# Kernel tuning notes

Measured on AMD Instinct MI355X. Metric: run time of the kernel, lower is better.

## Reference

```python
import jax, jax.numpy as jnp
import numpy as np

TEMPERATURE = 0.07
EPS = 1e-12  # matches torch F.normalize eps
B, D = 16384, 128


def setup_inputs() -> dict:
    key = jax.random.key(0)
    k1, k2 = jax.random.split(key)
    anchor = jax.random.normal(k1, (B, D), dtype=jnp.float32)
    positive = jax.random.normal(k2, (B, D), dtype=jnp.float32)
    return {"anchor": anchor, "positive": positive}


def _l2_normalize(x):
    # torch F.normalize: x / max(||x||, eps)
    n = jnp.sqrt(jnp.sum(x * x, axis=-1, keepdims=True))
    return x / jnp.maximum(n, EPS)


def reference(anchor, positive):
    a = _l2_normalize(anchor)          # [B, D]
    p = _l2_normalize(positive)        # [B, D]
    pos_sim = jnp.sum(a * p, axis=-1) / TEMPERATURE            # [B]
    sim = jnp.matmul(a, p.T) / TEMPERATURE                     # [B, B]
    neg_inf = jnp.finfo(sim.dtype).min
    bsz = sim.shape[0]
    eye = jnp.eye(bsz, dtype=bool)
    neg_sim = jnp.where(eye, neg_inf, sim)                     # diag masked
    logits = jnp.concatenate([pos_sim[:, None], neg_sim], axis=1)  # [B, B+1]
    # cross-entropy with label 0: -log_softmax(logits)[:, 0]
    lse = jax.nn.logsumexp(logits, axis=1)
    loss = lse - logits[:, 0]
    return jnp.mean(loss)
```

## Files before the change

kernel.cpp:

```cpp
#include <hip/hip_runtime.h>
#include <stdint.h>

#define NROWS 16384
#define DIM 128

typedef __attribute__((ext_vector_type(8))) __bf16 bf16x8;
typedef __attribute__((ext_vector_type(4))) float f32x4;
typedef __attribute__((ext_vector_type(4))) unsigned int u32x4;

constexpr float TEMP_INV = 1.0f / 0.07f;
constexpr float LOG2E = 1.4426950408889634f;
constexpr float LN2 = 0.69314718055994531f;
constexpr float KAPPA = LOG2E * TEMP_INV;
constexpr float SQRT_KAPPA = 4.53981600f;

__device__ __forceinline__ ushort f2bf(float x) {
  uint32_t u = __builtin_bit_cast(uint32_t, x);
  uint32_t r = (u + 0x7fffu + ((u >> 16) & 1u)) >> 16;
  return (ushort)r;
}

__device__ __forceinline__ void gload_lds16(const void* g, void* l) {
  __builtin_amdgcn_global_load_lds(
      (const __attribute__((address_space(1))) unsigned int*)g,
      (__attribute__((address_space(3))) unsigned int*)l, 16, 0, 0);
}

__global__ __launch_bounds__(256) void prep_kernel(
    const float* __restrict__ anchor, const float* __restrict__ positive,
    ushort* __restrict__ abar, ushort* __restrict__ pbar,
    float* __restrict__ pos_u)
{
  const int tid = threadIdx.x;
  const int row = blockIdx.x * 16 + (tid >> 4);
  const int c0 = (tid & 15) * 8;

  const float4* a4 = reinterpret_cast<const float4*>(anchor + (size_t)row * DIM + c0);
  const float4* p4 = reinterpret_cast<const float4*>(positive + (size_t)row * DIM + c0);
  float4 a0 = a4[0], a1 = a4[1];
  float4 p0 = p4[0], p1 = p4[1];

  float af[8] = {a0.x, a0.y, a0.z, a0.w, a1.x, a1.y, a1.z, a1.w};
  float pf[8] = {p0.x, p0.y, p0.z, p0.w, p1.x, p1.y, p1.z, p1.w};

  float sa = 0.f, sp = 0.f, dp = 0.f;
#pragma unroll
  for (int j = 0; j < 8; ++j) {
    sa += af[j] * af[j];
    sp += pf[j] * pf[j];
    dp += af[j] * pf[j];
  }
#pragma unroll
  for (int m = 1; m <= 8; m <<= 1) {
    sa += __shfl_xor(sa, m, 64);
    sp += __shfl_xor(sp, m, 64);
    dp += __shfl_xor(dp, m, 64);
  }
  float inva = 1.0f / fmaxf(sqrtf(sa), 1e-12f);
  float invp = 1.0f / fmaxf(sqrtf(sp), 1e-12f);
  float ca = inva * SQRT_KAPPA;
  float cp = invp * SQRT_KAPPA;

  ushort ua[8], up[8];
#pragma unroll
  for (int j = 0; j < 8; ++j) {
    ua[j] = f2bf(af[j] * ca);
    up[j] = f2bf(pf[j] * cp);
  }
  *reinterpret_cast<uint4*>(abar + (size_t)row * DIM + c0) = *reinterpret_cast<uint4*>(ua);
  *reinterpret_cast<uint4*>(pbar + (size_t)row * DIM + c0) = *reinterpret_cast<uint4*>(up);

  if ((tid & 15) == 0)
    pos_u[row] = dp * inva * invp * KAPPA;
}

#define NSPLIT 16
#define BM 256
#define CPB (NROWS / NSPLIT)
#define BN 32
#define NIT (CPB / BN)
#define NBUF 4
#define TILE_B (BN * 256)

__global__ __launch_bounds__(256, 4) void lse_kernel(
    const ushort* __restrict__ abar,
    const ushort* __restrict__ pbar,
    float* __restrict__ sbuf )
{
  __shared__ alignas(16) char lds[NBUF][TILE_B];

  const int tid = threadIdx.x;
  const int l = tid & 63;
  const int w = tid >> 6;
  const int r15 = l & 15;
  const int hi = l >> 4;

  const int bid = blockIdx.x;
  const int csplit = bid & 15;
  const int rowblk = bid >> 4;
  const int row0 = rowblk * BM + w * 64;
  const int col0 = csplit * CPB;

  const char* abase = (const char*)abar;
  const char* pbase = (const char*)pbar;

  bf16x8 afrag[4][4];
#pragma unroll
  for (int rg = 0; rg < 4; ++rg)
#pragma unroll
    for (int kk = 0; kk < 4; ++kk) {
      size_t off = (size_t)(row0 + rg * 16 + r15) * 256 + (size_t)(kk * 32 + hi * 8) * 2;
      u32x4 v = *reinterpret_cast<const u32x4*>(abase + off);
      afrag[rg][kk] = __builtin_bit_cast(bf16x8, v);
    }

  float s[4][4];
#pragma unroll
  for (int rg = 0; rg < 4; ++rg)
#pragma unroll
    for (int rr = 0; rr < 4; ++rr) s[rg][rr] = 0.f;

  const int trow = tid >> 4;
  const size_t src0 = (size_t)(col0 + trow) * 256 + (size_t)(((tid & 15) ^ (trow & 7)) * 16);
  char* const lds0 = &lds[0][0] + w * 1024;

#define STAGE(t)                                                              \
  do {                                                                        \
    const char* gsrc = pbase + src0 + (size_t)(t) * TILE_B;                   \
    char* ld = lds0 + (size_t)((t) & 3) * TILE_B;                             \
    gload_lds16(gsrc, ld);                                                    \
    gload_lds16(gsrc + 4096, ld + 4096);                                      \
  } while (0)

  STAGE(0);
  __builtin_amdgcn_sched_barrier(0);
  STAGE(1);
  __builtin_amdgcn_sched_barrier(0);

  for (int it = 0; it < NIT; ++it) {
    if (it < NIT - 1) {
      asm volatile("s_waitcnt vmcnt(2)" ::: "memory");
    } else {
      asm volatile("s_waitcnt vmcnt(0)" ::: "memory");
    }
    __builtin_amdgcn_s_barrier();
    asm volatile("" ::: "memory");
    __builtin_amdgcn_sched_barrier(0);

    if (it + 2 < NIT) STAGE(it + 2);

    const char* bufp = &lds[0][0] + (size_t)(it & 3) * TILE_B;
#pragma unroll
    for (int ctg = 0; ctg < 2; ++ctg) {
      const int tr = ctg * 16 + r15;
      const int sw = (tr & 7) << 4;
      const char* base = bufp + tr * 256;
      bf16x8 bfrag[4];
#pragma unroll
      for (int kk = 0; kk < 4; ++kk) {
        const int cb = kk * 64 + hi * 16;
        u32x4 v = *reinterpret_cast<const u32x4*>(base + (cb ^ sw));
        bfrag[kk] = __builtin_bit_cast(bf16x8, v);
      }
      __builtin_amdgcn_s_setprio(1);
#pragma unroll
      for (int rg = 0; rg < 4; ++rg) {
        f32x4 acc = {0.f, 0.f, 0.f, 0.f};
#pragma unroll
        for (int kk = 0; kk < 4; ++kk)
          acc = __builtin_amdgcn_mfma_f32_16x16x32_bf16(afrag[rg][kk], bfrag[kk], acc, 0, 0, 0);
        s[rg][0] += __builtin_amdgcn_exp2f(acc[0]);
        s[rg][1] += __builtin_amdgcn_exp2f(acc[1]);
        s[rg][2] += __builtin_amdgcn_exp2f(acc[2]);
        s[rg][3] += __builtin_amdgcn_exp2f(acc[3]);
      }
      __builtin_amdgcn_s_setprio(0);
    }
  }
#undef STAGE

#pragma unroll
  for (int rg = 0; rg < 4; ++rg)
#pragma unroll
    for (int rr = 0; rr < 4; ++rr) {
      float v = s[rg][rr];
      v += __shfl_xor(v, 1, 64);
      v += __shfl_xor(v, 2, 64);
      v += __shfl_xor(v, 4, 64);
      v += __shfl_xor(v, 8, 64);
      if (r15 == 0) {
        int grow = row0 + rg * 16 + hi * 4 + rr;
        sbuf[(size_t)csplit * NROWS + grow] = v;
      }
    }
}

__global__ __launch_bounds__(256) void finalize1(
    const float* __restrict__ sbuf, const float* __restrict__ pos_u,
    float* __restrict__ partial)
{
  const int tid = threadIdx.x;
  const int r = blockIdx.x * 256 + tid;
  float ssum = 0.f;
#pragma unroll
  for (int c = 0; c < NSPLIT; ++c) ssum += sbuf[(size_t)c * NROWS + r];
  float acc = LN2 * (__builtin_amdgcn_logf(ssum) - pos_u[r]);
#pragma unroll
  for (int m = 1; m <= 32; m <<= 1) acc += __shfl_xor(acc, m, 64);
  __shared__ float red[4];
  if ((tid & 63) == 0) red[tid >> 6] = acc;
  __syncthreads();
  if (tid == 0) partial[blockIdx.x] = red[0] + red[1] + red[2] + red[3];
}

__global__ __launch_bounds__(64) void finalize2(
    const float* __restrict__ partial, float* __restrict__ out)
{
  float v = partial[threadIdx.x];
#pragma unroll
  for (int m = 1; m <= 32; m <<= 1) v += __shfl_xor(v, m, 64);
  if (threadIdx.x == 0) out[0] = v * (1.0f / (float)NROWS);
}

extern "C" void kernel_launch(void* const* d_in, const int* in_sizes, int n_in,
                              void* d_out, int out_size, void* d_ws, size_t ws_size,
                              hipStream_t stream) {
  const float* anchor = (const float*)d_in[0];
  const float* positive = (const float*)d_in[1];
  char* ws = (char*)d_ws;

  ushort* abar = (ushort*)ws;
  ushort* pbar = (ushort*)(ws + (size_t)NROWS * DIM * 2);
  float* pos_u = (float*)(ws + (size_t)NROWS * DIM * 4);
  float* sbuf = (float*)(ws + (size_t)NROWS * DIM * 4 + (size_t)NROWS * 4);
  float* partial = (float*)(ws + (size_t)NROWS * DIM * 4 + (size_t)NROWS * 4
                            + (size_t)NSPLIT * NROWS * 4);
  float* out = (float*)d_out;

  prep_kernel<<<NROWS / 16, 256, 0, stream>>>(anchor, positive, abar, pbar, pos_u);
  lse_kernel<<<NSPLIT * (NROWS / BM), 256, 0, stream>>>(abar, pbar, sbuf);
  finalize1<<<NROWS / 256, 256, 0, stream>>>(sbuf, pos_u, partial);
  finalize2<<<1, 64, 0, stream>>>(partial, out);
}
```

Measured before the change: 87.59 us.

## Load B fragments directly from global into registers, dropping LDS staging

Removes the LDS ring buffer with its async global-to-LDS loads and per-iteration barriers. Each wave now reads its own B-operand fragments straight from global memory into registers, double-buffered in software, so loads overlap the MFMA and exp work. The four waves of a block no longer share a tile, so each wave re-reads the same columns through the cache, and launch bounds drop to 3 blocks per CU to leave room for the extra registers.

```diff
diff --git a/kernel.cpp b/kernel.cpp
--- a/kernel.cpp
+++ b/kernel.cpp
@@ -20,12 +20,6 @@
   return (ushort)r;
 }
 
-__device__ __forceinline__ void gload_lds16(const void* g, void* l) {
-  __builtin_amdgcn_global_load_lds(
-      (const __attribute__((address_space(1))) unsigned int*)g,
-      (__attribute__((address_space(3))) unsigned int*)l, 16, 0, 0);
-}
-
 __global__ __launch_bounds__(256) void prep_kernel(
     const float* __restrict__ anchor, const float* __restrict__ positive,
     ushort* __restrict__ abar, ushort* __restrict__ pbar,
@@ -79,16 +73,12 @@
 #define CPB (NROWS / NSPLIT)
 #define BN 32
 #define NIT (CPB / BN)
-#define NBUF 4
-#define TILE_B (BN * 256)
-
-__global__ __launch_bounds__(256, 4) void lse_kernel(
+
+__global__ __launch_bounds__(256, 3) void lse_kernel(
     const ushort* __restrict__ abar,
     const ushort* __restrict__ pbar,
     float* __restrict__ sbuf )
 {
-  __shared__ alignas(16) char lds[NBUF][TILE_B];
-
   const int tid = threadIdx.x;
   const int l = tid & 63;
   const int w = tid >> 6;
@@ -120,64 +110,42 @@
 #pragma unroll
     for (int rr = 0; rr < 4; ++rr) s[rg][rr] = 0.f;
 
-  const int trow = tid >> 4;
-  const size_t src0 = (size_t)(col0 + trow) * 256 + (size_t)(((tid & 15) ^ (trow & 7)) * 16);
-  char* const lds0 = &lds[0][0] + w * 1024;
-
-#define STAGE(t)                                                              \
-  do {                                                                        \
-    const char* gsrc = pbase + src0 + (size_t)(t) * TILE_B;                   \
-    char* ld = lds0 + (size_t)((t) & 3) * TILE_B;                             \
-    gload_lds16(gsrc, ld);                                                    \
-    gload_lds16(gsrc + 4096, ld + 4096);                                      \
-  } while (0)
-
-  STAGE(0);
-  __builtin_amdgcn_sched_barrier(0);
-  STAGE(1);
-  __builtin_amdgcn_sched_barrier(0);
-
-  for (int it = 0; it < NIT; ++it) {
-    if (it < NIT - 1) {
-      asm volatile("s_waitcnt vmcnt(2)" ::: "memory");
-    } else {
-      asm volatile("s_waitcnt vmcnt(0)" ::: "memory");
+  const char* bptr = pbase + (size_t)(col0 + r15) * 256 + (size_t)(hi * 16);
+
+  u32x4 b0[4], b1[4];
+
+  auto LOADH = [&](u32x4 (&buf)[4], int byteoff) {
+#pragma unroll
+    for (int kk = 0; kk < 4; ++kk)
+      buf[kk] = *reinterpret_cast<const u32x4*>(bptr + byteoff + kk * 64);
+  };
+  auto COMP = [&](u32x4 (&buf)[4]) {
+#pragma unroll
+    for (int rg = 0; rg < 4; ++rg) {
+      f32x4 acc = {0.f, 0.f, 0.f, 0.f};
+#pragma unroll
+      for (int kk = 0; kk < 4; ++kk)
+        acc = __builtin_amdgcn_mfma_f32_16x16x32_bf16(
+            afrag[rg][kk], __builtin_bit_cast(bf16x8, buf[kk]), acc, 0, 0, 0);
+      s[rg][0] += __builtin_amdgcn_exp2f(acc[0]);
+      s[rg][1] += __builtin_amdgcn_exp2f(acc[1]);
+      s[rg][2] += __builtin_amdgcn_exp2f(acc[2]);
+      s[rg][3] += __builtin_amdgcn_exp2f(acc[3]);
     }
-    __builtin_amdgcn_s_barrier();
-    asm volatile("" ::: "memory");
-    __builtin_amdgcn_sched_barrier(0);
-
-    if (it + 2 < NIT) STAGE(it + 2);
-
-    const char* bufp = &lds[0][0] + (size_t)(it & 3) * TILE_B;
-#pragma unroll
-    for (int ctg = 0; ctg < 2; ++ctg) {
-      const int tr = ctg * 16 + r15;
-      const int sw = (tr & 7) << 4;
-      const char* base = bufp + tr * 256;
-      bf16x8 bfrag[4];
-#pragma unroll
-      for (int kk = 0; kk < 4; ++kk) {
-        const int cb = kk * 64 + hi * 16;
-        u32x4 v = *reinterpret_cast<const u32x4*>(base + (cb ^ sw));
-        bfrag[kk] = __builtin_bit_cast(bf16x8, v);
-      }
-      __builtin_amdgcn_s_setprio(1);
-#pragma unroll
-      for (int rg = 0; rg < 4; ++rg) {
-        f32x4 acc = {0.f, 0.f, 0.f, 0.f};
-#pragma unroll
-        for (int kk = 0; kk < 4; ++kk)
-          acc = __builtin_amdgcn_mfma_f32_16x16x32_bf16(afrag[rg][kk], bfrag[kk], acc, 0, 0, 0);
-        s[rg][0] += __builtin_amdgcn_exp2f(acc[0]);
-        s[rg][1] += __builtin_amdgcn_exp2f(acc[1]);
-        s[rg][2] += __builtin_amdgcn_exp2f(acc[2]);
-        s[rg][3] += __builtin_amdgcn_exp2f(acc[3]);
-      }
-      __builtin_amdgcn_s_setprio(0);
-    }
-  }
-#undef STAGE
+  };
+
+  LOADH(b0, 0);
+  for (int it2 = 0; it2 < NIT; it2 += 2) {
+    LOADH(b1, 4096);
+    COMP(b0);
+    LOADH(b0, 8192);
+    COMP(b1);
+    LOADH(b1, 12288);
+    COMP(b0);
+    if (it2 + 2 < NIT) LOADH(b0, 16384);
+    COMP(b1);
+    bptr += 16384;
+  }
 
 #pragma unroll
   for (int rg = 0; rg < 4; ++rg)
```

Result: slower. 170.3 us (+94.4%).
